# Performance work log

Hardware: AMD Instinct MI355X
Metric: run time of the kernel (lower is better)

## Reference

```python
import jax, jax.numpy as jnp
import numpy as np
import math

INPUT_DIM = 1024
DIM_K = 1024
DIM_V = 1024
B, N = 4, 2048

def setup_inputs() -> dict:
    key = jax.random.key(0)
    ks = jax.random.split(key, 7)
    s = 1.0 / math.sqrt(INPUT_DIM)
    return {
        'x':  jax.random.normal(ks[0], (B, N, INPUT_DIM), dtype=jnp.float32),
        'Wq': jax.random.uniform(ks[1], (DIM_K, INPUT_DIM), jnp.float32, -s, s),
        'bq': jax.random.uniform(ks[2], (DIM_K,), jnp.float32, -s, s),
        'Wk': jax.random.uniform(ks[3], (DIM_K, INPUT_DIM), jnp.float32, -s, s),
        'bk': jax.random.uniform(ks[4], (DIM_K,), jnp.float32, -s, s),
        'Wv': jax.random.uniform(ks[5], (DIM_V, INPUT_DIM), jnp.float32, -s, s),
        'bv': jax.random.uniform(ks[6], (DIM_V,), jnp.float32, -s, s),
    }

def reference(x, Wq, bq, Wk, bk, Wv, bv):
    norm_fact = 1.0 / math.sqrt(DIM_K)
    # torch Linear: y = x @ W.T + b
    Q = jnp.einsum('bnd,kd->bnk', x, Wq) + bq  # [B,N,dim_k]
    K = jnp.einsum('bnd,kd->bnk', x, Wk) + bk  # [B,N,dim_k]
    V = jnp.einsum('bnd,vd->bnv', x, Wv) + bv  # [B,N,dim_v]
    scores = jnp.einsum('bqk,bnk->bqn', Q, K)  # [B,N,N]
    # NOTE: original code applies softmax FIRST, then scales by norm_fact
    atten = jax.nn.softmax(scores, axis=-1) * norm_fact
    return jnp.einsum('bqn,bnv->bqv', atten, V)  # [B,N,dim_v]
```

## Files before the change

### kernel.cpp

```cpp
#include <hip/hip_runtime.h>


typedef _Float16 hfx8 __attribute__((ext_vector_type(8)));
typedef _Float16 hfx4 __attribute__((ext_vector_type(4)));
typedef float fx4 __attribute__((ext_vector_type(4)));

__device__ __forceinline__ void load_lds16(const void* g, void* l) {
    __builtin_amdgcn_global_load_lds(
        (const __attribute__((address_space(1))) void*)g,
        (__attribute__((address_space(3))) void*)l, 16, 0, 0);
}

template <int N> __device__ __forceinline__ void vmwait() {
    if constexpr (N == 8) asm volatile("s_waitcnt vmcnt(8)" ::: "memory");
    else if constexpr (N == 6) asm volatile("s_waitcnt vmcnt(6)" ::: "memory");
    else asm volatile("s_waitcnt vmcnt(0)" ::: "memory");
}

__device__ __forceinline__ void xcd_remap(int& x, int& y, int& z) {
    const int gx = gridDim.x, gy = gridDim.y;
    const int lin = blockIdx.x + gx * (blockIdx.y + gy * blockIdx.z);
    const int cpx = (gx * gy * gridDim.z) >> 3;
    const int w = (lin & 7) * cpx + (lin >> 3);
    x = w % gx;
    y = (w / gx) % gy;
    z = w / (gx * gy);
}

__global__ __launch_bounds__(256) void conv_all_kernel(
    const float4* __restrict__ x, _Float16* __restrict__ xs,
    const float4* __restrict__ w0, const float4* __restrict__ w1, const float4* __restrict__ w2,
    _Float16* __restrict__ o0, _Float16* __restrict__ o1, _Float16* __restrict__ o2)
{
    const int b = blockIdx.x;
    const float4* in;
    _Float16* out;
    long i;
    if (b < 8192) {
        in = x; out = xs;
        i = (long)b * 256 + threadIdx.x;
    } else {
        const int wi = b - 8192;
        const int wsel = wi >> 10;
        in = wsel == 0 ? w0 : (wsel == 1 ? w1 : w2);
        out = wsel == 0 ? o0 : (wsel == 1 ? o1 : o2);
        i = (long)(wi & 1023) * 256 + threadIdx.x;
    }
    float4 v = in[i];
    hfx4 h;
    h[0] = (_Float16)v.x; h[1] = (_Float16)v.y;
    h[2] = (_Float16)v.z; h[3] = (_Float16)v.w;
    *(hfx4*)&out[i * 4] = h;
}

__global__ __launch_bounds__(256, 2) void gemmQKV(
    const _Float16* __restrict__ A,
    const _Float16* __restrict__ Bq, const _Float16* __restrict__ Bk, const _Float16* __restrict__ Bv,
    const float* __restrict__ bq, const float* __restrict__ bk, const float* __restrict__ bv,
    _Float16* __restrict__ oQ, _Float16* __restrict__ oK, _Float16* __restrict__ oV)
{
    constexpr int BK = 32;
    __shared__ __attribute__((aligned(16))) _Float16 lds[2][4 * 128 * BK];

    int bx, by, zz;
    xcd_remap(bx, by, zz);

    const int tid = threadIdx.x;
    const int lane = tid & 63;
    const int wv = tid >> 6;
    const int wr = wv >> 1, wc = wv & 1;
    const int lr = lane & 15, lk = lane >> 4;

    const long m0 = (long)by * 128;
    const long n0 = (long)bx * 128;

    fx4 acc[3][4][4] = {};

    auto STAGE = [&](int kt, int b) {
#pragma unroll
        for (int i = 0; i < 8; ++i) {
            const int slot = tid & 3;
            if (i < 2) {
                const int row = i * 64 + (tid >> 2);
                load_lds16(A + (m0 + row) * 1024L + kt + ((slot ^ ((row >> 1) & 3)) << 3),
                           &lds[b][row * BK + slot * 8]);
            } else {
                const int which = (i - 2) >> 1;
                const int row = ((i - 2) & 1) * 64 + (tid >> 2);
                const _Float16* Bsel = which == 0 ? Bq : (which == 1 ? Bk : Bv);
                load_lds16(Bsel + (n0 + row) * 1024L + kt + ((slot ^ ((row >> 1) & 3)) << 3),
                           &lds[b][(1 + which) * 4096 + row * BK + slot * 8]);
            }
        }
    };

    const int NT = 32;
    STAGE(0, 0);
    STAGE(BK, 1);
    vmwait<8>();
    __builtin_amdgcn_s_barrier();
    __builtin_amdgcn_sched_barrier(0);

    const int rA0 = wr * 64 + lr;
    const int rB0 = wc * 64 + lr;
    const int eA = (((rA0 >> 1) & 3) << 3);
    const int eB = (((rB0 >> 1) & 3) << 3);

    for (int t = 0; t < NT; ++t) {
        const _Float16* L = &lds[t & 1][0];

        hfx8 afr[4];
#pragma unroll
        for (int q = 0; q < 4; ++q)
            afr[q] = *(const hfx8*)&L[(rA0 + q * 16) * BK + ((lk * 8) ^ eA)];

#pragma unroll
        for (int w3 = 0; w3 < 3; ++w3) {
            hfx8 bfr[4];
#pragma unroll
            for (int nf = 0; nf < 4; ++nf)
                bfr[nf] = *(const hfx8*)&L[(1 + w3) * 4096 + (rB0 + nf * 16) * BK + ((lk * 8) ^ eB)];
            __builtin_amdgcn_s_setprio(1);
#pragma unroll
            for (int q = 0; q < 4; ++q)
#pragma unroll
                for (int nf = 0; nf < 4; ++nf)
                    acc[w3][q][nf] = __builtin_amdgcn_mfma_f32_16x16x32_f16(
                        afr[q], bfr[nf], acc[w3][q][nf], 0, 0, 0);
            __builtin_amdgcn_s_setprio(0);
        }

        __builtin_amdgcn_s_barrier();
        if (t + 2 < NT) {
            STAGE((t + 2) * BK, t & 1);
            vmwait<8>();
        } else {
            vmwait<0>();
        }
        __builtin_amdgcn_s_barrier();
        __builtin_amdgcn_sched_barrier(0);
    }

#pragma unroll
    for (int w3 = 0; w3 < 3; ++w3) {
#pragma unroll
        for (int mf = 0; mf < 4; ++mf) {
#pragma unroll
            for (int nf = 0; nf < 4; ++nf) {
                const long row0 = m0 + wr * 64 + mf * 16 + lk * 4;
                const long col = n0 + wc * 64 + nf * 16 + lr;
                if (w3 == 0) {
                    const float bb = bq[col];
#pragma unroll
                    for (int j = 0; j < 4; ++j)
                        oQ[(row0 + j) * 1024 + col] = (_Float16)(acc[0][mf][nf][j] + bb);
                } else if (w3 == 1) {
                    const float bb = bk[col];
#pragma unroll
                    for (int j = 0; j < 4; ++j)
                        oK[(row0 + j) * 1024 + col] = (_Float16)(acc[1][mf][nf][j] + bb);
                } else {
                    const float bb = bv[col];
                    hfx4 pk;
#pragma unroll
                    for (int j = 0; j < 4; ++j) pk[j] = (_Float16)(acc[2][mf][nf][j] + bb);
                    *(hfx4*)&oV[((row0 >> 11) * 1024 + col) * 2048 + (row0 & 2047)] = pk;
                }
            }
        }
    }
}

template <int OMODE>
__global__ __launch_bounds__(256, 2) void gemmS(
    const _Float16* __restrict__ A, const _Float16* __restrict__ B0,
    float* __restrict__ outF, _Float16* __restrict__ oH,
    int K, int lda, int ldb, int ldc, float alpha,
    long sAz, long sBz, long sCz)
{
    constexpr int BK = 32;
    __shared__ __attribute__((aligned(16))) _Float16 lds[2][384 * BK];

    int bx, by, z;
    xcd_remap(bx, by, z);

    A += (long)z * sAz;
    const _Float16* B = B0 + (long)z * sBz;

    const int tid = threadIdx.x;
    const int lane = tid & 63;
    const int wv = tid >> 6;
    const int wr = wv >> 1, wc = wv & 1;
    const int lr = lane & 15, lk = lane >> 4;

    const long m0 = (long)by * 128;
    const long n0 = (long)bx * 256;

    fx4 acc[2][4][4] = {};

    auto STAGE = [&](int kt, int b) {
#pragma unroll
        for (int i = 0; i < 6; ++i) {
            const int c = i * 256 + tid;
            const int slot = c & 3;
            if (i < 2) {
                const int row = c >> 2;
                load_lds16(A + (m0 + row) * (long)lda + kt + ((slot ^ ((row >> 1) & 3)) << 3),
                           &lds[b][row * BK + slot * 8]);
            } else {
                const int c2 = c - 512;
                const int row = c2 >> 2;
                load_lds16(B + (n0 + row) * (long)ldb + kt + ((slot ^ ((row >> 1) & 3)) << 3),
                           &lds[b][4096 + row * BK + slot * 8]);
            }
        }
    };

    const int NT = K / BK;
    STAGE(0, 0);
    STAGE(BK, 1);
    vmwait<6>();
    __builtin_amdgcn_s_barrier();
    __builtin_amdgcn_sched_barrier(0);

    const int rA0 = wr * 64 + lr;
    const int rB0 = wc * 64 + lr;
    const int eA = (((rA0 >> 1) & 3) << 3);
    const int eB = (((rB0 >> 1) & 3) << 3);

    for (int t = 0; t < NT; ++t) {
        const _Float16* L = &lds[t & 1][0];

        hfx8 afr[4];
#pragma unroll
        for (int q = 0; q < 4; ++q)
            afr[q] = *(const hfx8*)&L[(rA0 + q * 16) * BK + ((lk * 8) ^ eA)];

#pragma unroll
        for (int s = 0; s < 2; ++s) {
            hfx8 bfr[4];
#pragma unroll
            for (int nf = 0; nf < 4; ++nf)
                bfr[nf] = *(const hfx8*)&L[4096 + s * 4096 + (rB0 + nf * 16) * BK + ((lk * 8) ^ eB)];
            __builtin_amdgcn_s_setprio(1);
#pragma unroll
            for (int q = 0; q < 4; ++q)
#pragma unroll
                for (int nf = 0; nf < 4; ++nf)
                    acc[s][q][nf] = __builtin_amdgcn_mfma_f32_16x16x32_f16(
                        afr[q], bfr[nf], acc[s][q][nf], 0, 0, 0);
            __builtin_amdgcn_s_setprio(0);
        }

        __builtin_amdgcn_s_barrier();
        if (t + 2 < NT) {
            STAGE((t + 2) * BK, t & 1);
            vmwait<6>();
        } else {
            vmwait<0>();
        }
        __builtin_amdgcn_s_barrier();
        __builtin_amdgcn_sched_barrier(0);
    }

#pragma unroll
    for (int s = 0; s < 2; ++s) {
#pragma unroll
        for (int mf = 0; mf < 4; ++mf) {
#pragma unroll
            for (int nf = 0; nf < 4; ++nf) {
                const long row0 = m0 + wr * 64 + mf * 16 + lk * 4;
                const long col = n0 + s * 128 + wc * 64 + nf * 16 + lr;
                if constexpr (OMODE == 0) {
                    float* oz = outF + (long)z * sCz;
#pragma unroll
                    for (int j = 0; j < 4; ++j)
                        oz[(row0 + j) * (long)ldc + col] = alpha * acc[s][mf][nf][j];
                } else {
                    _Float16* oz = oH + (long)z * sCz;
#pragma unroll
                    for (int j = 0; j < 4; ++j)
                        oz[(row0 + j) * (long)ldc + col] = (_Float16)(alpha * acc[s][mf][nf][j]);
                }
            }
        }
    }
}

__global__ __launch_bounds__(256) void softmax_kernel(_Float16* __restrict__ S)
{
    const long row = blockIdx.x;
    _Float16* r = S + row * 2048;
    const int t = threadIdx.x;

    const hfx8 hv = *(const hfx8*)&r[t * 8];
    float v[8];
#pragma unroll
    for (int j = 0; j < 8; ++j) v[j] = (float)hv[j];

    float mx = v[0];
#pragma unroll
    for (int j = 1; j < 8; ++j) mx = fmaxf(mx, v[j]);
#pragma unroll
    for (int o = 32; o; o >>= 1) mx = fmaxf(mx, __shfl_xor(mx, o, 64));

    __shared__ float redm[4];
    __shared__ float reds[4];
    const int w = t >> 6;
    if ((t & 63) == 0) redm[w] = mx;
    __syncthreads();
    mx = fmaxf(fmaxf(redm[0], redm[1]), fmaxf(redm[2], redm[3]));

    float e[8];
    float s = 0.f;
#pragma unroll
    for (int j = 0; j < 8; ++j) {
        e[j] = __expf(v[j] - mx);
        s += e[j];
    }
#pragma unroll
    for (int o = 32; o; o >>= 1) s += __shfl_xor(s, o, 64);
    if ((t & 63) == 0) reds[w] = s;
    __syncthreads();
    s = reds[0] + reds[1] + reds[2] + reds[3];

    const float inv = 1.0f / s;
    hfx8 p;
#pragma unroll
    for (int j = 0; j < 8; ++j) p[j] = (_Float16)(e[j] * inv);
    *(hfx8*)&r[t * 8] = p;
}

extern "C" void kernel_launch(void* const* d_in, const int* in_sizes, int n_in,
                              void* d_out, int out_size, void* d_ws, size_t ws_size,
                              hipStream_t stream)
{
    const float* x  = (const float*)d_in[0];
    const float* Wq = (const float*)d_in[1];
    const float* bq = (const float*)d_in[2];
    const float* Wk = (const float*)d_in[3];
    const float* bk = (const float*)d_in[4];
    const float* Wv = (const float*)d_in[5];
    const float* bv = (const float*)d_in[6];
    float* out = (float*)d_out;

    _Float16* xs  = (_Float16*)d_ws;
    _Float16* Wqh = xs + 8192ull * 1024;
    _Float16* Wkh = Wqh + 1024ull * 1024;
    _Float16* Wvh = Wkh + 1024ull * 1024;
    _Float16* Qp  = Wvh + 1024ull * 1024;
    _Float16* Ks  = Qp + 8192ull * 1024;
    _Float16* Vt  = Ks + 8192ull * 1024;
    _Float16* Sh  = Vt + 4ull * 1024 * 2048;

    dim3 blk(256);

    conv_all_kernel<<<11264, blk, 0, stream>>>(
        (const float4*)x, xs,
        (const float4*)Wq, (const float4*)Wk, (const float4*)Wv, Wqh, Wkh, Wvh);

    gemmQKV<<<dim3(8, 64, 1), blk, 0, stream>>>(
        xs, Wqh, Wkh, Wvh, bq, bk, bv, Qp, Ks, Vt);

    gemmS<2><<<dim3(8, 16, 4), blk, 0, stream>>>(
        Qp, Ks, nullptr, Sh,
        1024, 1024, 1024, 2048, 1.0f,
        2097152L, 2097152L, 4194304L);

    softmax_kernel<<<2048 * 4, blk, 0, stream>>>(Sh);

    gemmS<0><<<dim3(4, 16, 4), blk, 0, stream>>>(
        Sh, Vt, out, nullptr,
        2048, 2048, 2048, 1024, 0.03125f,
        4194304L, 2097152L, 2097152L);
}
```

Before: 168.7 us.

## Widen batched GEMM tiles to three 128-column strips per block

The S=QK^T and PV GEMMs now give each block up to three 128-wide N strips (128x384 tile) instead of two (128x256), which shrinks the grid and increases A-tile reuse. The last block in each row handles a partial set of strips, clamping its loads and skipping MFMA work for missing strips. The grids become 384 and 192 blocks, under 2 per CU on 256 CUs, so the risk is poor occupancy, load imbalance from partial blocks, and higher register pressure from the larger accumulator array.

```diff
diff --git a/kernel.cpp b/kernel.cpp
--- a/kernel.cpp
+++ b/kernel.cpp
@@ -13,7 +13,6 @@
 
 template <int N> __device__ __forceinline__ void vmwait() {
     if constexpr (N == 8) asm volatile("s_waitcnt vmcnt(8)" ::: "memory");
-    else if constexpr (N == 6) asm volatile("s_waitcnt vmcnt(6)" ::: "memory");
     else asm volatile("s_waitcnt vmcnt(0)" ::: "memory");
 }
 
@@ -172,20 +171,23 @@
 }
 
 template <int OMODE>
-__global__ __launch_bounds__(256, 2) void gemmS(
+__global__ __launch_bounds__(256, 2) void gemmMS(
     const _Float16* __restrict__ A, const _Float16* __restrict__ B0,
     float* __restrict__ outF, _Float16* __restrict__ oH,
     int K, int lda, int ldb, int ldc, float alpha,
-    long sAz, long sBz, long sCz)
+    long sAz, long sBz, long sCz, int NSTRIPS)
 {
     constexpr int BK = 32;
-    __shared__ __attribute__((aligned(16))) _Float16 lds[2][384 * BK];
+    __shared__ __attribute__((aligned(16))) _Float16 lds[2][4 * 128 * BK];
 
     int bx, by, z;
     xcd_remap(bx, by, z);
 
     A += (long)z * sAz;
     const _Float16* B = B0 + (long)z * sBz;
+
+    const int base = bx * 3;
+    const int ns = min(3, NSTRIPS - base);
 
     const int tid = threadIdx.x;
     const int lane = tid & 63;
@@ -194,24 +196,23 @@
     const int lr = lane & 15, lk = lane >> 4;
 
     const long m0 = (long)by * 128;
-    const long n0 = (long)bx * 256;
-
-    fx4 acc[2][4][4] = {};
+
+    fx4 acc[3][4][4] = {};
 
     auto STAGE = [&](int kt, int b) {
 #pragma unroll
-        for (int i = 0; i < 6; ++i) {
-            const int c = i * 256 + tid;
-            const int slot = c & 3;
+        for (int i = 0; i < 8; ++i) {
+            const int slot = tid & 3;
             if (i < 2) {
-                const int row = c >> 2;
+                const int row = i * 64 + (tid >> 2);
                 load_lds16(A + (m0 + row) * (long)lda + kt + ((slot ^ ((row >> 1) & 3)) << 3),
                            &lds[b][row * BK + slot * 8]);
             } else {
-                const int c2 = c - 512;
-                const int row = c2 >> 2;
-                load_lds16(B + (n0 + row) * (long)ldb + kt + ((slot ^ ((row >> 1) & 3)) << 3),
-                           &lds[b][4096 + row * BK + slot * 8]);
+                const int which = (i - 2) >> 1;
+                const int row = ((i - 2) & 1) * 64 + (tid >> 2);
+                const int strip = min(base + which, NSTRIPS - 1);
+                load_lds16(B + ((long)strip * 128 + row) * (long)ldb + kt + ((slot ^ ((row >> 1) & 3)) << 3),
+                           &lds[b][(1 + which) * 4096 + row * BK + slot * 8]);
             }
         }
     };
@@ -219,7 +220,7 @@
     const int NT = K / BK;
     STAGE(0, 0);
     STAGE(BK, 1);
-    vmwait<6>();
+    vmwait<8>();
     __builtin_amdgcn_s_barrier();
     __builtin_amdgcn_sched_barrier(0);
 
@@ -237,25 +238,27 @@
             afr[q] = *(const hfx8*)&L[(rA0 + q * 16) * BK + ((lk * 8) ^ eA)];
 
 #pragma unroll
-        for (int s = 0; s < 2; ++s) {
-            hfx8 bfr[4];
-#pragma unroll
-            for (int nf = 0; nf < 4; ++nf)
-                bfr[nf] = *(const hfx8*)&L[4096 + s * 4096 + (rB0 + nf * 16) * BK + ((lk * 8) ^ eB)];
-            __builtin_amdgcn_s_setprio(1);
-#pragma unroll
-            for (int q = 0; q < 4; ++q)
+        for (int s = 0; s < 3; ++s) {
+            if (s < ns) {
+                hfx8 bfr[4];
 #pragma unroll
                 for (int nf = 0; nf < 4; ++nf)
-                    acc[s][q][nf] = __builtin_amdgcn_mfma_f32_16x16x32_f16(
-                        afr[q], bfr[nf], acc[s][q][nf], 0, 0, 0);
-            __builtin_amdgcn_s_setprio(0);
+                    bfr[nf] = *(const hfx8*)&L[(1 + s) * 4096 + (rB0 + nf * 16) * BK + ((lk * 8) ^ eB)];
+                __builtin_amdgcn_s_setprio(1);
+#pragma unroll
+                for (int q = 0; q < 4; ++q)
+#pragma unroll
+                    for (int nf = 0; nf < 4; ++nf)
+                        acc[s][q][nf] = __builtin_amdgcn_mfma_f32_16x16x32_f16(
+                            afr[q], bfr[nf], acc[s][q][nf], 0, 0, 0);
+                __builtin_amdgcn_s_setprio(0);
+            }
         }
 
         __builtin_amdgcn_s_barrier();
         if (t + 2 < NT) {
             STAGE((t + 2) * BK, t & 1);
-            vmwait<6>();
+            vmwait<8>();
         } else {
             vmwait<0>();
         }
@@ -264,23 +267,25 @@
     }
 
 #pragma unroll
-    for (int s = 0; s < 2; ++s) {
-#pragma unroll
-        for (int mf = 0; mf < 4; ++mf) {
-#pragma unroll
-            for (int nf = 0; nf < 4; ++nf) {
-                const long row0 = m0 + wr * 64 + mf * 16 + lk * 4;
-                const long col = n0 + s * 128 + wc * 64 + nf * 16 + lr;
-                if constexpr (OMODE == 0) {
-                    float* oz = outF + (long)z * sCz;
-#pragma unroll
-                    for (int j = 0; j < 4; ++j)
-                        oz[(row0 + j) * (long)ldc + col] = alpha * acc[s][mf][nf][j];
-                } else {
-                    _Float16* oz = oH + (long)z * sCz;
-#pragma unroll
-                    for (int j = 0; j < 4; ++j)
-                        oz[(row0 + j) * (long)ldc + col] = (_Float16)(alpha * acc[s][mf][nf][j]);
+    for (int s = 0; s < 3; ++s) {
+        if (s < ns) {
+#pragma unroll
+            for (int mf = 0; mf < 4; ++mf) {
+#pragma unroll
+                for (int nf = 0; nf < 4; ++nf) {
+                    const long row0 = m0 + wr * 64 + mf * 16 + lk * 4;
+                    const long col = (long)(base + s) * 128 + wc * 64 + nf * 16 + lr;
+                    if constexpr (OMODE == 0) {
+                        float* oz = outF + (long)z * sCz;
+#pragma unroll
+                        for (int j = 0; j < 4; ++j)
+                            oz[(row0 + j) * (long)ldc + col] = alpha * acc[s][mf][nf][j];
+                    } else {
+                        _Float16* oz = oH + (long)z * sCz;
+#pragma unroll
+                        for (int j = 0; j < 4; ++j)
+                            oz[(row0 + j) * (long)ldc + col] = (_Float16)(alpha * acc[s][mf][nf][j]);
+                    }
                 }
             }
         }
@@ -362,15 +367,15 @@
     gemmQKV<<<dim3(8, 64, 1), blk, 0, stream>>>(
         xs, Wqh, Wkh, Wvh, bq, bk, bv, Qp, Ks, Vt);
 
-    gemmS<2><<<dim3(8, 16, 4), blk, 0, stream>>>(
+    gemmMS<2><<<dim3(6, 16, 4), blk, 0, stream>>>(
         Qp, Ks, nullptr, Sh,
         1024, 1024, 1024, 2048, 1.0f,
-        2097152L, 2097152L, 4194304L);
+        2097152L, 2097152L, 4194304L, 16);
 
     softmax_kernel<<<2048 * 4, blk, 0, stream>>>(Sh);
 
-    gemmS<0><<<dim3(4, 16, 4), blk, 0, stream>>>(
+    gemmMS<0><<<dim3(3, 16, 4), blk, 0, stream>>>(
         Sh, Vt, out, nullptr,
         2048, 2048, 2048, 1024, 0.03125f,
-        4194304L, 2097152L, 2097152L);
-}
+        4194304L, 2097152L, 2097152L, 8);
+}
```

After: 185.6 us. +10.0%, slower.
